# Kernel tuning notes

Measured on AMD Instinct MI355X. Metric: run time of the kernel, lower is better.

The kernel has to match this reference:

```python
import jax, jax.numpy as jnp
import numpy as np

B, T, I, H, L = 32, 2048, 256, 512, 2

def setup_inputs() -> dict:
    key = jax.random.key(0)
    ks = jax.random.split(key, 6)
    s_i = 1.0 / np.sqrt(I)
    s_h = 1.0 / np.sqrt(H)
    return {
        "x": jax.random.normal(ks[0], (B, T, I), dtype=jnp.float32),
        "W_ih0": jax.random.normal(ks[1], (I, H), dtype=jnp.float32) * s_i,
        "W_hh0": jax.random.normal(ks[2], (H, H), dtype=jnp.float32) * s_h,
        "b0": jnp.zeros((H,), dtype=jnp.float32),
        "W_ih1": jax.random.normal(ks[3], (H, H), dtype=jnp.float32) * s_h,
        "W_hh1": jax.random.normal(ks[4], (H, H), dtype=jnp.float32) * s_h,
        "b1": jnp.zeros((H,), dtype=jnp.float32),
    }

def reference(x, W_ih0, W_hh0, b0, W_ih1, W_hh1, b1):
    # Multi-layer Elman-tanh RNN: h_j = tanh(in @ W_ih + h_j @ W_hh + b); out == h.
    params = ((W_ih0, W_hh0, b0), (W_ih1, W_hh1, b1))
    b, h = x.shape[0], W_hh0.shape[0]
    h0 = jnp.zeros((len(params), b, h), dtype=x.dtype)  # hidden=None -> zeros

    def step(hid, xt):
        out = xt
        new_h = []
        for j, (Wi, Wh, bj) in enumerate(params):
            hj = jnp.tanh(out @ Wi + hid[j] @ Wh + bj)
            new_h.append(hj)
            out = hj
        return jnp.stack(new_h), out

    hT, ys = jax.lax.scan(step, h0, jnp.swapaxes(x, 0, 1))  # ys: [T, B, H]
    out = jnp.swapaxes(ys, 0, 1)  # [B, T, H]
    return out, hT
```

## Files before the change

kernel.cpp:

```cpp
#include <hip/hip_runtime.h>
#include <math.h>

#define TT 2048
#define BB 32
#define HH 512

template<int K>
__global__ void __launch_bounds__(256)
ih_gemm(const float* X, const float* __restrict__ W,
        const float* __restrict__ bias, float* OUT)
{
    __shared__ float xt[32][K];
    const int wg  = (int)blockIdx.x;
    const int tid = (int)threadIdx.x;
    const long row0 = (long)wg * 32;

    {
        const float4* Xv = (const float4*)(X + row0 * K);
        float4* xtv = (float4*)(&xt[0][0]);
        const int n4 = 8 * K;
        for (int i = tid; i < n4; i += 256) xtv[i] = Xv[i];
    }
    __syncthreads();

    const int j2 = tid * 2;
    float acc0[32], acc1[32];
    #pragma unroll
    for (int r = 0; r < 32; ++r) { acc0[r] = 0.f; acc1[r] = 0.f; }

    for (int k = 0; k < K; k += 4) {
        const float2 w0 = *(const float2*)&W[(k+0)*HH + j2];
        const float2 w1 = *(const float2*)&W[(k+1)*HH + j2];
        const float2 w2 = *(const float2*)&W[(k+2)*HH + j2];
        const float2 w3 = *(const float2*)&W[(k+3)*HH + j2];
        #pragma unroll
        for (int r = 0; r < 32; ++r) {
            const float4 xv = *(const float4*)&xt[r][k];
            acc0[r] += xv.x*w0.x + xv.y*w1.x + xv.z*w2.x + xv.w*w3.x;
            acc1[r] += xv.x*w0.y + xv.y*w1.y + xv.z*w2.y + xv.w*w3.y;
        }
    }
    const float2 bv = *(const float2*)&bias[j2];
    #pragma unroll
    for (int r = 0; r < 32; ++r) {
        float2 o; o.x = acc0[r] + bv.x; o.y = acc1[r] + bv.y;
        *(float2*)&OUT[(row0 + r) * HH + j2] = o;
    }
}

static __device__ __forceinline__ float tanhx(float s) {
    const float e = __expf(2.0f * s);
    return 1.0f - 2.0f / (e + 1.0f);
}
static __device__ __forceinline__ void pub(unsigned long long* p, unsigned tag, float v) {
    __hip_atomic_store(p, ((unsigned long long)tag << 32) | (unsigned long long)__float_as_uint(v),
                       __ATOMIC_RELAXED, __HIP_MEMORY_SCOPE_AGENT);
}
static __device__ __forceinline__ float pollv(unsigned long long* p, unsigned want) {
    unsigned long long pk = __hip_atomic_load(p, __ATOMIC_RELAXED, __HIP_MEMORY_SCOPE_AGENT);
    while ((unsigned)(pk >> 32) != want)
        pk = __hip_atomic_load(p, __ATOMIC_RELAXED, __HIP_MEMORY_SCOPE_AGENT);
    return __uint_as_float((unsigned)(pk & 0xffffffffu));
}

__global__ void __attribute__((amdgpu_flat_work_group_size(512, 512),
                               amdgpu_waves_per_eu(2, 2)))
fused_recur(const float* __restrict__ Whh0, const float* __restrict__ Wih1,
            const float* __restrict__ Whh1, const float* __restrict__ b1,
            float* __restrict__ seq, float* __restrict__ hTout,
            unsigned long long* __restrict__ hb0, unsigned long long* __restrict__ hb1)
{
    __shared__ float lds_a[2][8][64];
    __shared__ float lds_b[2][8][64];
    const int bid  = (int)blockIdx.x;
    const int c    = bid & 31;
    const int x    = bid >> 5;
    const int tid  = (int)threadIdx.x;
    const int lane = tid & 63;
    const int w    = tid >> 6;
    const int J    = (x << 6) + lane;
    const long wb  = (long)(w << 6) * HH + J;

    float4 wa0,wa1,wa2,wa3,wa4,wa5,wa6,wa7,wa8,wa9,wa10,wa11,wa12,wa13,wa14,wa15;
    float4 wi0,wi1,wi2,wi3,wi4,wi5,wi6,wi7,wi8,wi9,wi10,wi11,wi12,wi13,wi14,wi15;
    float4 wh0,wh1,wh2,wh3,wh4,wh5,wh6,wh7,wh8,wh9,wh10,wh11,wh12,wh13,wh14,wh15;
#define LD1(P, M, q) do { \
        P##q.x = M[wb + (4*q+0)*HH]; P##q.y = M[wb + (4*q+1)*HH]; \
        P##q.z = M[wb + (4*q+2)*HH]; P##q.w = M[wb + (4*q+3)*HH]; } while (0)
#define LD16(P, M) do { LD1(P,M,0); LD1(P,M,1); LD1(P,M,2); LD1(P,M,3); \
        LD1(P,M,4); LD1(P,M,5); LD1(P,M,6); LD1(P,M,7); LD1(P,M,8); LD1(P,M,9); \
        LD1(P,M,10); LD1(P,M,11); LD1(P,M,12); LD1(P,M,13); LD1(P,M,14); LD1(P,M,15); } while (0)
    LD16(wa, Whh0); LD16(wi, Wih1); LD16(wh, Whh1);
#undef LD16
#undef LD1
#define PIN1(P, q) asm volatile("" : "+v"(P##q.x), "+v"(P##q.y), "+v"(P##q.z), "+v"(P##q.w))
#define PIN16(P) do { PIN1(P,0); PIN1(P,1); PIN1(P,2); PIN1(P,3); PIN1(P,4); PIN1(P,5); \
        PIN1(P,6); PIN1(P,7); PIN1(P,8); PIN1(P,9); PIN1(P,10); PIN1(P,11); PIN1(P,12); \
        PIN1(P,13); PIN1(P,14); PIN1(P,15); } while (0)
    PIN16(wa); PIN16(wi); PIN16(wh);
#undef PIN16
#undef PIN1

    unsigned long long* hbc0 = hb0 + c * (2 * HH);
    unsigned long long* hbc1 = hb1 + c * (2 * HH);
    float* rowbase = seq + (long)c * TT * HH;

    float pre_cur = 0.f, b1v = 0.f;
    if (tid < 64) { pre_cur = rowbase[J]; b1v = b1[J]; }

    if (tid < 64) {
        const float hv = tanhx(pre_cur);
        pub(hbc0 + J, 1u, hv);
        pre_cur = rowbase[HH + J];
    }
    float h1reg = 0.f;

    for (int t = 0; t < TT; ++t) {
        const float h0new = pollv(hbc0 + ((t & 1) << 9) + (w << 6) + lane, (unsigned)(t + 1));
        const unsigned h0bits = __float_as_uint(h0new);

        if (t + 1 < TT) {
            float a0 = 0.f, a1 = 0.f, a2 = 0.f, a3 = 0.f;
#define BC0(i) __uint_as_float(__builtin_amdgcn_readlane(h0bits, (i)))
#define MACA(q) do { a0 = fmaf(BC0(4*q+0), wa##q.x, a0); a1 = fmaf(BC0(4*q+1), wa##q.y, a1); \
                     a2 = fmaf(BC0(4*q+2), wa##q.z, a2); a3 = fmaf(BC0(4*q+3), wa##q.w, a3); } while (0)
            MACA(0); MACA(1); MACA(2); MACA(3); MACA(4); MACA(5); MACA(6); MACA(7);
            MACA(8); MACA(9); MACA(10); MACA(11); MACA(12); MACA(13); MACA(14); MACA(15);
#undef MACA
            lds_a[(t + 1) & 1][w][lane] = (a0 + a1) + (a2 + a3);
            __syncthreads();
            if (tid < 64) {
                float s = pre_cur;
                #pragma unroll
                for (int q = 0; q < 8; ++q) s += lds_a[(t + 1) & 1][q][lane];
                const float hv = tanhx(s);
                pub(hbc0 + (((t + 1) & 1) << 9) + J, (unsigned)(t + 2), hv);
                if (t + 2 < TT) pre_cur = rowbase[(long)(t + 2) * HH + J];
                if (t + 1 == TT - 1) hTout[(c << 9) + J] = hv;
            }
        }

        if (t > 0)
            h1reg = pollv(hbc1 + (((t - 1) & 1) << 9) + (w << 6) + lane, (unsigned)t);
        const unsigned h1bits = __float_as_uint(h1reg);

        {
            float a0 = 0.f, a1 = 0.f, a2 = 0.f, a3 = 0.f;
#define BC1(i) __uint_as_float(__builtin_amdgcn_readlane(h1bits, (i)))
#define MACI(q) do { a0 = fmaf(BC0(4*q+0), wi##q.x, a0); a1 = fmaf(BC0(4*q+1), wi##q.y, a1); \
                     a2 = fmaf(BC0(4*q+2), wi##q.z, a2); a3 = fmaf(BC0(4*q+3), wi##q.w, a3); } while (0)
#define MACH(q) do { a0 = fmaf(BC1(4*q+0), wh##q.x, a0); a1 = fmaf(BC1(4*q+1), wh##q.y, a1); \
                     a2 = fmaf(BC1(4*q+2), wh##q.z, a2); a3 = fmaf(BC1(4*q+3), wh##q.w, a3); } while (0)
            MACI(0); MACI(1); MACI(2); MACI(3); MACI(4); MACI(5); MACI(6); MACI(7);
            MACI(8); MACI(9); MACI(10); MACI(11); MACI(12); MACI(13); MACI(14); MACI(15);
            MACH(0); MACH(1); MACH(2); MACH(3); MACH(4); MACH(5); MACH(6); MACH(7);
            MACH(8); MACH(9); MACH(10); MACH(11); MACH(12); MACH(13); MACH(14); MACH(15);
#undef MACH
#undef MACI
#undef BC1
#undef BC0
            lds_b[t & 1][w][lane] = (a0 + a1) + (a2 + a3);
            __syncthreads();
            if (tid < 64) {
                float s2 = b1v;
                #pragma unroll
                for (int q = 0; q < 8; ++q) s2 += lds_b[t & 1][q][lane];
                const float h1v = tanhx(s2);
                rowbase[(long)t * HH + J] = h1v;
                if (t + 1 < TT) pub(hbc1 + ((t & 1) << 9) + J, (unsigned)(t + 1), h1v);
                else hTout[(BB << 9) + (c << 9) + J] = h1v;
            }
        }
    }
}

extern "C" void kernel_launch(void* const* d_in, const int* in_sizes, int n_in,
                              void* d_out, int out_size, void* d_ws, size_t ws_size,
                              hipStream_t stream) {
    const float* x    = (const float*)d_in[0];
    const float* Wih0 = (const float*)d_in[1];
    const float* Whh0 = (const float*)d_in[2];
    const float* b0   = (const float*)d_in[3];
    const float* Wih1 = (const float*)d_in[4];
    const float* Whh1 = (const float*)d_in[5];
    const float* b1   = (const float*)d_in[6];

    float* out = (float*)d_out;
    float* hT  = out + (size_t)BB * TT * HH;

    unsigned long long* hb0 = (unsigned long long*)d_ws;
    unsigned long long* hb1 = hb0 + (size_t)BB * 2 * HH;
    (void)hipMemsetAsync(d_ws, 0, (size_t)2 * BB * 2 * HH * sizeof(unsigned long long), stream);

    ih_gemm<256><<<dim3((BB * TT) / 32), dim3(256), 0, stream>>>(x, Wih0, b0, out);
    fused_recur<<<dim3(256), dim3(512), 0, stream>>>(Whh0, Wih1, Whh1, b1,
                                                     out, hT, hb0, hb1);
}
```

Baseline: 4.285 ms.

## Interleave two batch rows per workgroup to hide cross-block polling latency

Each workgroup now processes two batch rows (c and c+16) in an interleaved schedule instead of one, halving the grid to 128 blocks. While one row's layer results propagate through global flags, the block computes the other row, and it non-blockingly samples the next needed flags ahead of time so the spin-wait is often skipped. Layer-1 finalization moves to wave 1 to spread the serial reduction work off wave 0. This doubles per-block serial work and uses half the CUs, and it trades that against lower effective synchronization latency.

```diff
diff --git a/kernel.cpp b/kernel.cpp
--- a/kernel.cpp
+++ b/kernel.cpp
@@ -62,24 +62,29 @@
         pk = __hip_atomic_load(p, __ATOMIC_RELAXED, __HIP_MEMORY_SCOPE_AGENT);
     return __uint_as_float((unsigned)(pk & 0xffffffffu));
 }
+static __device__ __forceinline__ unsigned long long samp(unsigned long long* p) {
+    return __hip_atomic_load(p, __ATOMIC_RELAXED, __HIP_MEMORY_SCOPE_AGENT);
+}
 
 __global__ void __attribute__((amdgpu_flat_work_group_size(512, 512),
                                amdgpu_waves_per_eu(2, 2)))
-fused_recur(const float* __restrict__ Whh0, const float* __restrict__ Wih1,
-            const float* __restrict__ Whh1, const float* __restrict__ b1,
-            float* __restrict__ seq, float* __restrict__ hTout,
-            unsigned long long* __restrict__ hb0, unsigned long long* __restrict__ hb1)
+fused_recur2(const float* __restrict__ Whh0, const float* __restrict__ Wih1,
+             const float* __restrict__ Whh1, const float* __restrict__ b1,
+             float* __restrict__ seq, float* __restrict__ hTout,
+             unsigned long long* __restrict__ hb0, unsigned long long* __restrict__ hb1)
 {
-    __shared__ float lds_a[2][8][64];
-    __shared__ float lds_b[2][8][64];
+    __shared__ float lds_aA[2][8][64], lds_bA[2][8][64];
+    __shared__ float lds_aB[2][8][64], lds_bB[2][8][64];
     const int bid  = (int)blockIdx.x;
-    const int c    = bid & 31;
-    const int x    = bid >> 5;
+    const int cA   = bid & 15;
+    const int cB   = cA + 16;
+    const int x    = bid >> 4;
     const int tid  = (int)threadIdx.x;
     const int lane = tid & 63;
     const int w    = tid >> 6;
     const int J    = (x << 6) + lane;
     const long wb  = (long)(w << 6) * HH + J;
+    const int slot = (w << 6) + lane;
 
     float4 wa0,wa1,wa2,wa3,wa4,wa5,wa6,wa7,wa8,wa9,wa10,wa11,wa12,wa13,wa14,wa15;
     float4 wi0,wi1,wi2,wi3,wi4,wi5,wi6,wi7,wi8,wi9,wi10,wi11,wi12,wi13,wi14,wi15;
@@ -101,77 +106,158 @@
 #undef PIN16
 #undef PIN1
 
-    unsigned long long* hbc0 = hb0 + c * (2 * HH);
-    unsigned long long* hbc1 = hb1 + c * (2 * HH);
-    float* rowbase = seq + (long)c * TT * HH;
-
-    float pre_cur = 0.f, b1v = 0.f;
-    if (tid < 64) { pre_cur = rowbase[J]; b1v = b1[J]; }
+    unsigned long long* hbc0A = hb0 + cA * (2 * HH);
+    unsigned long long* hbc1A = hb1 + cA * (2 * HH);
+    unsigned long long* hbc0B = hb0 + cB * (2 * HH);
+    unsigned long long* hbc1B = hb1 + cB * (2 * HH);
+    float* rowA = seq + (long)cA * TT * HH;
+    float* rowB = seq + (long)cB * TT * HH;
+
+    float preA = 0.f, preB = 0.f, b1v = 0.f;
+    if (tid < 64) { preA = rowA[J]; preB = rowB[J]; }
+    if (tid >= 64 && tid < 128) b1v = b1[J];
 
     if (tid < 64) {
-        const float hv = tanhx(pre_cur);
-        pub(hbc0 + J, 1u, hv);
-        pre_cur = rowbase[HH + J];
-    }
-    float h1reg = 0.f;
+        pub(hbc0A + J, 1u, tanhx(preA));
+        pub(hbc0B + J, 1u, tanhx(preB));
+        preA = rowA[HH + J];
+        preB = rowB[HH + J];
+    }
+    float h1A = 0.f, h1B = 0.f;
+    unsigned long long p3sA = 0, p3sB = 0, p2sA = 0, p2sB = 0;
+
+#define BCA0(i) __uint_as_float(__builtin_amdgcn_readlane(h0bitsA, (i)))
+#define BCA1(i) __uint_as_float(__builtin_amdgcn_readlane(h1bitsA, (i)))
+#define BCB0(i) __uint_as_float(__builtin_amdgcn_readlane(h0bitsB, (i)))
+#define BCB1(i) __uint_as_float(__builtin_amdgcn_readlane(h1bitsB, (i)))
 
     for (int t = 0; t < TT; ++t) {
-        const float h0new = pollv(hbc0 + ((t & 1) << 9) + (w << 6) + lane, (unsigned)(t + 1));
-        const unsigned h0bits = __float_as_uint(h0new);
+        float h0Av;
+        if ((unsigned)(p3sA >> 32) == (unsigned)(t + 1))
+            h0Av = __uint_as_float((unsigned)p3sA);
+        else
+            h0Av = pollv(hbc0A + ((t & 1) << 9) + slot, (unsigned)(t + 1));
+        const unsigned h0bitsA = __float_as_uint(h0Av);
+
+        if (t > 0) p2sA = samp(hbc1A + (((t - 1) & 1) << 9) + slot);
+        p3sB = samp(hbc0B + ((t & 1) << 9) + slot);
 
         if (t + 1 < TT) {
             float a0 = 0.f, a1 = 0.f, a2 = 0.f, a3 = 0.f;
-#define BC0(i) __uint_as_float(__builtin_amdgcn_readlane(h0bits, (i)))
-#define MACA(q) do { a0 = fmaf(BC0(4*q+0), wa##q.x, a0); a1 = fmaf(BC0(4*q+1), wa##q.y, a1); \
-                     a2 = fmaf(BC0(4*q+2), wa##q.z, a2); a3 = fmaf(BC0(4*q+3), wa##q.w, a3); } while (0)
+#define MACA(q) do { a0 = fmaf(BCA0(4*q+0), wa##q.x, a0); a1 = fmaf(BCA0(4*q+1), wa##q.y, a1); \
+                     a2 = fmaf(BCA0(4*q+2), wa##q.z, a2); a3 = fmaf(BCA0(4*q+3), wa##q.w, a3); } while (0)
             MACA(0); MACA(1); MACA(2); MACA(3); MACA(4); MACA(5); MACA(6); MACA(7);
             MACA(8); MACA(9); MACA(10); MACA(11); MACA(12); MACA(13); MACA(14); MACA(15);
 #undef MACA
-            lds_a[(t + 1) & 1][w][lane] = (a0 + a1) + (a2 + a3);
+            lds_aA[(t + 1) & 1][w][lane] = (a0 + a1) + (a2 + a3);
             __syncthreads();
             if (tid < 64) {
-                float s = pre_cur;
-                #pragma unroll
-                for (int q = 0; q < 8; ++q) s += lds_a[(t + 1) & 1][q][lane];
+                float s = preA;
+                #pragma unroll
+                for (int q = 0; q < 8; ++q) s += lds_aA[(t + 1) & 1][q][lane];
                 const float hv = tanhx(s);
-                pub(hbc0 + (((t + 1) & 1) << 9) + J, (unsigned)(t + 2), hv);
-                if (t + 2 < TT) pre_cur = rowbase[(long)(t + 2) * HH + J];
-                if (t + 1 == TT - 1) hTout[(c << 9) + J] = hv;
-            }
-        }
-
-        if (t > 0)
-            h1reg = pollv(hbc1 + (((t - 1) & 1) << 9) + (w << 6) + lane, (unsigned)t);
-        const unsigned h1bits = __float_as_uint(h1reg);
-
+                pub(hbc0A + (((t + 1) & 1) << 9) + J, (unsigned)(t + 2), hv);
+                if (t + 2 < TT) preA = rowA[(long)(t + 2) * HH + J];
+                if (t + 1 == TT - 1) hTout[(cA << 9) + J] = hv;
+            }
+        }
+        if (t > 0) {
+            if ((unsigned)(p2sA >> 32) == (unsigned)t)
+                h1A = __uint_as_float((unsigned)p2sA);
+            else
+                h1A = pollv(hbc1A + (((t - 1) & 1) << 9) + slot, (unsigned)t);
+        }
+        const unsigned h1bitsA = __float_as_uint(h1A);
         {
             float a0 = 0.f, a1 = 0.f, a2 = 0.f, a3 = 0.f;
-#define BC1(i) __uint_as_float(__builtin_amdgcn_readlane(h1bits, (i)))
-#define MACI(q) do { a0 = fmaf(BC0(4*q+0), wi##q.x, a0); a1 = fmaf(BC0(4*q+1), wi##q.y, a1); \
-                     a2 = fmaf(BC0(4*q+2), wi##q.z, a2); a3 = fmaf(BC0(4*q+3), wi##q.w, a3); } while (0)
-#define MACH(q) do { a0 = fmaf(BC1(4*q+0), wh##q.x, a0); a1 = fmaf(BC1(4*q+1), wh##q.y, a1); \
-                     a2 = fmaf(BC1(4*q+2), wh##q.z, a2); a3 = fmaf(BC1(4*q+3), wh##q.w, a3); } while (0)
+#define MACI(q) do { a0 = fmaf(BCA0(4*q+0), wi##q.x, a0); a1 = fmaf(BCA0(4*q+1), wi##q.y, a1); \
+                     a2 = fmaf(BCA0(4*q+2), wi##q.z, a2); a3 = fmaf(BCA0(4*q+3), wi##q.w, a3); } while (0)
+#define MACH(q) do { a0 = fmaf(BCA1(4*q+0), wh##q.x, a0); a1 = fmaf(BCA1(4*q+1), wh##q.y, a1); \
+                     a2 = fmaf(BCA1(4*q+2), wh##q.z, a2); a3 = fmaf(BCA1(4*q+3), wh##q.w, a3); } while (0)
             MACI(0); MACI(1); MACI(2); MACI(3); MACI(4); MACI(5); MACI(6); MACI(7);
             MACI(8); MACI(9); MACI(10); MACI(11); MACI(12); MACI(13); MACI(14); MACI(15);
             MACH(0); MACH(1); MACH(2); MACH(3); MACH(4); MACH(5); MACH(6); MACH(7);
             MACH(8); MACH(9); MACH(10); MACH(11); MACH(12); MACH(13); MACH(14); MACH(15);
 #undef MACH
 #undef MACI
-#undef BC1
-#undef BC0
-            lds_b[t & 1][w][lane] = (a0 + a1) + (a2 + a3);
+            lds_bA[t & 1][w][lane] = (a0 + a1) + (a2 + a3);
+            __syncthreads();
+            if (tid >= 64 && tid < 128) {
+                float s2 = b1v;
+                #pragma unroll
+                for (int q = 0; q < 8; ++q) s2 += lds_bA[t & 1][q][lane];
+                const float h1v = tanhx(s2);
+                rowA[(long)t * HH + J] = h1v;
+                if (t + 1 < TT) pub(hbc1A + ((t & 1) << 9) + J, (unsigned)(t + 1), h1v);
+                else hTout[(BB << 9) + (cA << 9) + J] = h1v;
+            }
+        }
+
+        float h0Bv;
+        if ((unsigned)(p3sB >> 32) == (unsigned)(t + 1))
+            h0Bv = __uint_as_float((unsigned)p3sB);
+        else
+            h0Bv = pollv(hbc0B + ((t & 1) << 9) + slot, (unsigned)(t + 1));
+        const unsigned h0bitsB = __float_as_uint(h0Bv);
+
+        if (t > 0) p2sB = samp(hbc1B + (((t - 1) & 1) << 9) + slot);
+        if (t + 1 < TT) p3sA = samp(hbc0A + (((t + 1) & 1) << 9) + slot);
+
+        if (t + 1 < TT) {
+            float a0 = 0.f, a1 = 0.f, a2 = 0.f, a3 = 0.f;
+#define MACA(q) do { a0 = fmaf(BCB0(4*q+0), wa##q.x, a0); a1 = fmaf(BCB0(4*q+1), wa##q.y, a1); \
+                     a2 = fmaf(BCB0(4*q+2), wa##q.z, a2); a3 = fmaf(BCB0(4*q+3), wa##q.w, a3); } while (0)
+            MACA(0); MACA(1); MACA(2); MACA(3); MACA(4); MACA(5); MACA(6); MACA(7);
+            MACA(8); MACA(9); MACA(10); MACA(11); MACA(12); MACA(13); MACA(14); MACA(15);
+#undef MACA
+            lds_aB[(t + 1) & 1][w][lane] = (a0 + a1) + (a2 + a3);
             __syncthreads();
             if (tid < 64) {
+                float s = preB;
+                #pragma unroll
+                for (int q = 0; q < 8; ++q) s += lds_aB[(t + 1) & 1][q][lane];
+                const float hv = tanhx(s);
+                pub(hbc0B + (((t + 1) & 1) << 9) + J, (unsigned)(t + 2), hv);
+                if (t + 2 < TT) preB = rowB[(long)(t + 2) * HH + J];
+                if (t + 1 == TT - 1) hTout[(cB << 9) + J] = hv;
+            }
+        }
+        if (t > 0) {
+            if ((unsigned)(p2sB >> 32) == (unsigned)t)
+                h1B = __uint_as_float((unsigned)p2sB);
+            else
+                h1B = pollv(hbc1B + (((t - 1) & 1) << 9) + slot, (unsigned)t);
+        }
+        const unsigned h1bitsB = __float_as_uint(h1B);
+        {
+            float a0 = 0.f, a1 = 0.f, a2 = 0.f, a3 = 0.f;
+#define MACI(q) do { a0 = fmaf(BCB0(4*q+0), wi##q.x, a0); a1 = fmaf(BCB0(4*q+1), wi##q.y, a1); \
+                     a2 = fmaf(BCB0(4*q+2), wi##q.z, a2); a3 = fmaf(BCB0(4*q+3), wi##q.w, a3); } while (0)
+#define MACH(q) do { a0 = fmaf(BCB1(4*q+0), wh##q.x, a0); a1 = fmaf(BCB1(4*q+1), wh##q.y, a1); \
+                     a2 = fmaf(BCB1(4*q+2), wh##q.z, a2); a3 = fmaf(BCB1(4*q+3), wh##q.w, a3); } while (0)
+            MACI(0); MACI(1); MACI(2); MACI(3); MACI(4); MACI(5); MACI(6); MACI(7);
+            MACI(8); MACI(9); MACI(10); MACI(11); MACI(12); MACI(13); MACI(14); MACI(15);
+            MACH(0); MACH(1); MACH(2); MACH(3); MACH(4); MACH(5); MACH(6); MACH(7);
+            MACH(8); MACH(9); MACH(10); MACH(11); MACH(12); MACH(13); MACH(14); MACH(15);
+#undef MACH
+#undef MACI
+            lds_bB[t & 1][w][lane] = (a0 + a1) + (a2 + a3);
+            __syncthreads();
+            if (tid >= 64 && tid < 128) {
                 float s2 = b1v;
                 #pragma unroll
-                for (int q = 0; q < 8; ++q) s2 += lds_b[t & 1][q][lane];
+                for (int q = 0; q < 8; ++q) s2 += lds_bB[t & 1][q][lane];
                 const float h1v = tanhx(s2);
-                rowbase[(long)t * HH + J] = h1v;
-                if (t + 1 < TT) pub(hbc1 + ((t & 1) << 9) + J, (unsigned)(t + 1), h1v);
-                else hTout[(BB << 9) + (c << 9) + J] = h1v;
-            }
-        }
-    }
+                rowB[(long)t * HH + J] = h1v;
+                if (t + 1 < TT) pub(hbc1B + ((t & 1) << 9) + J, (unsigned)(t + 1), h1v);
+                else hTout[(BB << 9) + (cB << 9) + J] = h1v;
+            }
+        }
+    }
+#undef BCB1
+#undef BCB0
+#undef BCA1
+#undef BCA0
 }
 
 extern "C" void kernel_launch(void* const* d_in, const int* in_sizes, int n_in,
@@ -193,6 +279,6 @@
     (void)hipMemsetAsync(d_ws, 0, (size_t)2 * BB * 2 * HH * sizeof(unsigned long long), stream);
 
     ih_gemm<256><<<dim3((BB * TT) / 32), dim3(256), 0, stream>>>(x, Wih0, b0, out);
-    fused_recur<<<dim3(256), dim3(512), 0, stream>>>(Whh0, Wih1, Whh1, b1,
-                                                     out, hT, hb0, hb1);
-}
+    fused_recur2<<<dim3(128), dim3(512), 0, stream>>>(Whh0, Wih1, Whh1, b1,
+                                                      out, hT, hb0, hb1);
+}
```

Result: slower. 6.954 ms (+62.3%).
